# Optimization experiments

Hardware: AMD Instinct MI355X
Metric: run time of the kernel (lower is better)

Reference implementation:

```python
import jax, jax.numpy as jnp
import numpy as np

TIME_DIM = 2
DIM = 512
N_ENT = 100000
N_REL = 500
B = 512
K = 128
MARGIN = 2.0
EPS = 1e-6


def proj_tan0(u):
    # tangent space at origin o=(1,0,...,0): first coordinate zeroed
    return u.at[..., 0].set(0.0)


def expmap0(u):
    # exponential map at the origin of the pseudo-hyperboloid Q^{s,t}, beta=-1.
    # quadratic norm of tangent vector (time dims negative): branch on sign.
    u = proj_tan0(u)
    a = -jnp.sum(u[..., :TIME_DIM] ** 2, axis=-1) + jnp.sum(u[..., TIME_DIM:] ** 2, axis=-1)
    sp = jnp.sqrt(jnp.clip(a, EPS))   # space-like branch radius
    st = jnp.sqrt(jnp.clip(-a, EPS))  # time-like branch radius
    c = jnp.where(a > 0, jnp.cosh(sp), jnp.cos(st))
    s = jnp.where(a > 0, jnp.sinh(sp) / sp, jnp.sin(st) / st)
    o = jnp.zeros_like(u).at[..., 0].set(1.0)
    return c[..., None] * o + s[..., None] * u


def _norm_givens(r):
    g = r.reshape(r.shape[0], -1, 2)
    return g / jnp.clip(jnp.linalg.norm(g, axis=-1, keepdims=True), 1e-15)


def givens_rotations(r, x):
    g = _norm_givens(r)
    xp = x.reshape(r.shape[0], -1, 2)
    c, s = g[..., 0:1], g[..., 1:2]
    x0, x1 = xp[..., 0:1], xp[..., 1:2]
    out = jnp.concatenate([c * x0 - s * x1, c * x1 + s * x0], axis=-1)
    return out.reshape(r.shape[0], -1)


def givens_reflection(r, x):
    g = _norm_givens(r)
    xp = x.reshape(r.shape[0], -1, 2)
    c, s = g[..., 0:1], g[..., 1:2]
    x0, x1 = xp[..., 0:1], xp[..., 1:2]
    out = jnp.concatenate([c * x0 + s * x1, s * x0 - c * x1], axis=-1)
    return out.reshape(r.shape[0], -1)


def manhattan_sqdist(x, y):
    # Manhattan-style geodesic on Q^{s,t} via the S^{t-1} x H^s decomposition:
    # leg 1: rotate time direction on the sphere of radius ||x_t||,
    # leg 2: hyperbolic distance along the shared time direction. Asymmetric
    # in (x, y), hence the min over both orders in the caller.
    xt, xs = x[..., :TIME_DIM], x[..., TIME_DIM:]
    yt, ys = y[..., :TIME_DIM], y[..., TIME_DIM:]
    nx = jnp.linalg.norm(xt, axis=-1)
    ny = jnp.linalg.norm(yt, axis=-1)
    cosang = jnp.clip(jnp.sum(xt * yt, axis=-1) / (nx * ny), -1.0 + EPS, 1.0 - EPS)
    d_sph = nx * jnp.arccos(cosang)
    inner = nx * ny - jnp.sum(xs * ys, axis=-1)
    d_hyp = jnp.arccosh(jnp.clip(inner, 1.0 + EPS))
    return (d_sph + d_hyp) ** 2


def setup_inputs() -> dict:
    key = jax.random.key(0)
    ks = jax.random.split(key, 8)
    emb_entity = jax.random.normal(ks[0], (N_ENT, DIM), jnp.float32)
    relation_boost = 1e-5 * jax.nn.softplus(jax.random.normal(ks[1], (N_REL, TIME_DIM), jnp.float32))
    relation_rot_left = 2.0 * jax.random.uniform(ks[2], (N_REL, DIM), jnp.float32) - 1.0
    relation_rot_right = 2.0 * jax.random.uniform(ks[3], (N_REL, DIM), jnp.float32) - 1.0
    bias_head = jnp.zeros((N_ENT,), jnp.float32)
    bias_tail = jnp.zeros((N_ENT,), jnp.float32)
    u_idx = jax.random.randint(ks[4], (B,), 0, N_ENT)
    r_idx = jax.random.randint(ks[5], (B,), 0, N_REL)
    v_idx = jax.random.randint(ks[6], (B, K), 0, N_ENT)
    return {"emb_entity": emb_entity, "relation_boost": relation_boost,
            "relation_rot_left": relation_rot_left, "relation_rot_right": relation_rot_right,
            "bias_head": bias_head, "bias_tail": bias_tail,
            "u_idx": u_idx, "r_idx": r_idx, "v_idx": v_idx}


def reference(emb_entity, relation_boost, relation_rot_left, relation_rot_right,
              bias_head, bias_tail, u_idx, r_idx, v_idx):
    head = emb_entity[u_idx]                       # [B, D]
    tail = emb_entity[v_idx]                       # [B, K, D]
    b = jax.nn.softplus(relation_boost[r_idx])     # [B, 2]
    r_left = relation_rot_left[r_idx]
    r_right = relation_rot_right[r_idx]

    head = expmap0(head)
    tail = expmap0(proj_tan0(tail))

    head = givens_rotations(r_right, head)

    # dense (D x D) Lorentz boost per example, faithful to the original matmul
    C = jnp.sqrt(1.0 + b ** 2)
    t_idx = jnp.arange(TIME_DIM)
    bt_idx = DIM - TIME_DIM + jnp.arange(TIME_DIM)
    m_idx = jnp.arange(TIME_DIM, DIM - TIME_DIM)
    boost = jnp.zeros((b.shape[0], DIM, DIM), head.dtype)
    boost = boost.at[:, t_idx, t_idx].set(C)
    boost = boost.at[:, bt_idx, bt_idx].set(C)
    boost = boost.at[:, t_idx, bt_idx].set(-b)
    boost = boost.at[:, bt_idx, t_idx].set(-b)
    boost = boost.at[:, m_idx, m_idx].set(1.0)
    head = jnp.einsum('bij,bj->bi', boost, head)

    head = givens_reflection(r_left, head)

    # pairwise manifold distance, min over the two Manhattan-path orders
    c1 = manhattan_sqdist(head[:, None, :], tail)  # [B, K]
    c2 = manhattan_sqdist(tail, head[:, None, :])
    dist = jnp.minimum(c1, c2)

    return MARGIN - dist + bias_head[u_idx][:, None] + bias_tail[v_idx]
```

## Files before the change

kernel.cpp:

```cpp
#include <hip/hip_runtime.h>
#include <math.h>

#define DIM_ 512
#define K_ 128
#define EPS_ 1e-6f
#define MARGIN_ 2.0f
#define PI_ 3.14159265358979f
#define QSTRIDE 68

__device__ __forceinline__ float frcp(float x) { return __builtin_amdgcn_rcpf(x); }

__device__ __forceinline__ float fast_acos(float x) {
    float ax = fabsf(x);
    float p = -0.0187293f;
    p = p * ax + 0.0742610f;
    p = p * ax - 0.2121144f;
    p = p * ax + 1.5707288f;
    float r = sqrtf(fmaxf(1.f - ax, 0.f)) * p;
    return x < 0.f ? PI_ - r : r;
}

__device__ __forceinline__ void fast_coshsinh(float x, float& c, float& s) {
    float e  = __expf(x);
    float ei = frcp(e);
    c = 0.5f * (e + ei);
    s = 0.5f * (e - ei);
}

__device__ __forceinline__ void expmap_cs(float a, float& c, float& s) {
    if (a > 0.f) {
        float sp = sqrtf(fmaxf(a, EPS_));
        float ch, sh;
        fast_coshsinh(sp, ch, sh);
        c = ch; s = sh * frcp(sp);
    } else {
        float st = sqrtf(fmaxf(-a, EPS_));
        c = __cosf(st);
        s = __sinf(st) * frcp(st);
    }
}

__device__ __forceinline__ void givens_rot(float gc, float gs, float& x0, float& x1) {
    float rn = frcp(fmaxf(sqrtf(gc * gc + gs * gs), 1e-15f));
    float c = gc * rn, s = gs * rn;
    float y0 = c * x0 - s * x1;
    float y1 = c * x1 + s * x0;
    x0 = y0; x1 = y1;
}

__device__ __forceinline__ void givens_ref(float gc, float gs, float& x0, float& x1) {
    float rn = frcp(fmaxf(sqrtf(gc * gc + gs * gs), 1e-15f));
    float c = gc * rn, s = gs * rn;
    float y0 = c * x0 + s * x1;
    float y1 = s * x0 - c * x1;
    x0 = y0; x1 = y1;
}

__global__ __launch_bounds__(256) void ultrae_kernel(
    const float* __restrict__ emb,
    const float* __restrict__ rel_boost,
    const float* __restrict__ rot_left,
    const float* __restrict__ rot_right,
    const float* __restrict__ bias_head,
    const float* __restrict__ bias_tail,
    const int* __restrict__ u_idx,
    const int* __restrict__ r_idx,
    const int* __restrict__ v_idx,
    float* __restrict__ out)
{
    __shared__ float lds_q[4][8 * QSTRIDE + 4];
    __shared__ float lds_d[4][8 * QSTRIDE + 4];
    __shared__ float lds_t[4][8];

    const int b = blockIdx.x;
    const int lane = threadIdx.x & 63;
    const int wave = threadIdx.x >> 6;
    const int u = u_idx[b];
    const int r = r_idx[b];

    const int kbase = (blockIdx.y * 4 + wave) * 8;
    const int* vp = v_idx + b * K_ + kbase;
    const int4 vv0 = *(const int4*)(vp);
    const int4 vv1 = *(const int4*)(vp + 4);
    const int vi[8] = {vv0.x, vv0.y, vv0.z, vv0.w, vv1.x, vv1.y, vv1.z, vv1.w};
    float4 t0[8], t1[8];
#pragma unroll
    for (int j = 0; j < 8; ++j) {
        const float* trow = emb + (size_t)vi[j] * DIM_ + lane * 8;
        t0[j] = *(const float4*)trow;
        t1[j] = *(const float4*)(trow + 4);
    }

    const float* hrow = emb + (size_t)u * DIM_ + lane * 8;
    float4 h0 = *(const float4*)hrow;
    float4 h1 = *(const float4*)(hrow + 4);
    const float* rr = rot_right + (size_t)r * DIM_ + lane * 8;
    float4 gr0 = *(const float4*)rr;
    float4 gr1 = *(const float4*)(rr + 4);
    const float* rl = rot_left + (size_t)r * DIM_ + lane * 8;
    float4 gl0 = *(const float4*)rl;
    float4 gl1 = *(const float4*)(rl + 4);
    const float rb0 = rel_boost[2*r];
    const float rb1 = rel_boost[2*r+1];
    const float bh = bias_head[u];

    const int m = lane & 7;
    const int g = lane >> 3;
    float bt = 0.f;
    if (lane < 8) bt = bias_tail[vp[m]];

    if (lane == 0) h0.x = 0.f;
    float ps = h0.x*h0.x + h0.y*h0.y + h0.z*h0.z + h0.w*h0.w
             + h1.x*h1.x + h1.y*h1.y + h1.z*h1.z + h1.w*h1.w;
#pragma unroll
    for (int off = 32; off >= 1; off >>= 1) ps += __shfl_xor(ps, off, 64);
    float u1 = __shfl(h0.y, 0, 64);
    float a = ps - 2.f * u1 * u1;
    float ch, sh;
    expmap_cs(a, ch, sh);
    h0.x *= sh; h0.y *= sh; h0.z *= sh; h0.w *= sh;
    h1.x *= sh; h1.y *= sh; h1.z *= sh; h1.w *= sh;
    if (lane == 0) h0.x = ch;

    givens_rot(gr0.x, gr0.y, h0.x, h0.y);
    givens_rot(gr0.z, gr0.w, h0.z, h0.w);
    givens_rot(gr1.x, gr1.y, h1.x, h1.y);
    givens_rot(gr1.z, gr1.w, h1.z, h1.w);

    {
        float bb0 = __logf(1.f + __expf(rb0));
        float bb1 = __logf(1.f + __expf(rb1));
        float C0 = sqrtf(1.f + bb0*bb0);
        float C1 = sqrtf(1.f + bb1*bb1);
        float e0   = __shfl(h0.x, 0, 64);
        float e1   = __shfl(h0.y, 0, 64);
        float e510 = __shfl(h1.z, 63, 64);
        float e511 = __shfl(h1.w, 63, 64);
        if (lane == 0) {
            h0.x = C0*e0 - bb0*e510;
            h0.y = C1*e1 - bb1*e511;
        }
        if (lane == 63) {
            h1.z = C0*e510 - bb0*e0;
            h1.w = C1*e511 - bb1*e1;
        }
    }

    givens_ref(gl0.x, gl0.y, h0.x, h0.y);
    givens_ref(gl0.z, gl0.w, h0.z, h0.w);
    givens_ref(gl1.x, gl1.y, h1.x, h1.y);
    givens_ref(gl1.z, gl1.w, h1.z, h1.w);

    float hf0 = __shfl(h0.x, 0, 64);
    float hf1 = __shfl(h0.y, 0, 64);
    float nx = sqrtf(hf0*hf0 + hf1*hf1);
    if (lane == 0) { h0.x = 0.f; h0.y = 0.f; }
    const float rnx = frcp(nx);

    if (lane == 0) {
#pragma unroll
        for (int j = 0; j < 8; ++j) lds_t[wave][j] = t0[j].y;
    }

#pragma unroll
    for (int j = 0; j < 8; ++j) {
        float4 s0 = t0[j], s1 = t1[j];
        if (lane == 0) { s0.x = 0.f; s0.y = 0.f; }
        float qp = s0.x*s0.x + s0.y*s0.y + s0.z*s0.z + s0.w*s0.w
                 + s1.x*s1.x + s1.y*s1.y + s1.z*s1.z + s1.w*s1.w;
        float dp = h0.x*s0.x + h0.y*s0.y + h0.z*s0.z + h0.w*s0.w
                 + h1.x*s1.x + h1.y*s1.y + h1.z*s1.z + h1.w*s1.w;
        lds_q[wave][j * QSTRIDE + lane] = qp;
        lds_d[wave][j * QSTRIDE + lane] = dp;
    }

    __builtin_amdgcn_wave_barrier();

    float q = 0.f, d = 0.f;
    const float* qa = &lds_q[wave][m * QSTRIDE + g];
    const float* da = &lds_d[wave][m * QSTRIDE + g];
#pragma unroll
    for (int k = 0; k < 8; ++k) {
        q += qa[8 * k];
        d += da[8 * k];
    }
    q += __shfl_xor(q, 8, 64);  d += __shfl_xor(d, 8, 64);
    q += __shfl_xor(q, 16, 64); d += __shfl_xor(d, 16, 64);
    q += __shfl_xor(q, 32, 64); d += __shfl_xor(d, 32, 64);

    const float tt1 = lds_t[wave][m];

    float at = q - tt1 * tt1;
    float ct, st;
    expmap_cs(at, ct, st);
    float yt1 = st * tt1;
    float ny = sqrtf(ct*ct + yt1*yt1);
    float cosang = (hf0*ct + hf1*yt1) * rnx * frcp(ny);
    cosang = fminf(fmaxf(cosang, -1.f + EPS_), 1.f - EPS_);
    float dsph = fminf(nx, ny) * fast_acos(cosang);
    float inner = fmaxf(nx*ny - st*d, 1.f + EPS_);
    float dhyp = __logf(inner + sqrtf(inner - 1.f) * sqrtf(inner + 1.f));
    float dsum = dsph + dhyp;
    if (lane < 8) {
        out[b * K_ + kbase + m] = MARGIN_ - dsum*dsum + bh + bt;
    }
}

extern "C" void kernel_launch(void* const* d_in, const int* in_sizes, int n_in,
                              void* d_out, int out_size, void* d_ws, size_t ws_size,
                              hipStream_t stream) {
    const float* emb       = (const float*)d_in[0];
    const float* rel_boost = (const float*)d_in[1];
    const float* rot_left  = (const float*)d_in[2];
    const float* rot_right = (const float*)d_in[3];
    const float* bias_h    = (const float*)d_in[4];
    const float* bias_t    = (const float*)d_in[5];
    const int* u_idx       = (const int*)d_in[6];
    const int* r_idx       = (const int*)d_in[7];
    const int* v_idx       = (const int*)d_in[8];
    float* out = (float*)d_out;

    int B = in_sizes[6];
    dim3 grid(B, 4), block(256);
    hipLaunchKernelGGL(ultrae_kernel, grid, block, 0, stream,
                       emb, rel_boost, rot_left, rot_right,
                       bias_h, bias_t, u_idx, r_idx, v_idx, out);
}
```

Before: 272.7 us.

## Split head transform into a prep kernel and change per-lane element layout

The per-example head pipeline (expmap, Givens rotation, Lorentz boost, reflection) moves into a separate kernel that runs once per example. It writes the transformed head plus scalars (time components, norm, bias) to workspace, and the main kernel reads them. Before, each of the 16 waves handling an example recomputed the head. Lanes also now load two contiguous float4 chunks (offset lane*4 and +256) instead of eight adjacent floats, so each load instruction covers a contiguous span. The cost is an extra kernel launch and a workspace write/read round trip.

New measurement: 277.8 us. Within noise of the previous version (+1.9%).

```diff
diff --git a/kernel.cpp b/kernel.cpp
--- a/kernel.cpp
+++ b/kernel.cpp
@@ -7,6 +7,7 @@
 #define MARGIN_ 2.0f
 #define PI_ 3.14159265358979f
 #define QSTRIDE 68
+#define HSTRIDE 520
 
 __device__ __forceinline__ float frcp(float x) { return __builtin_amdgcn_rcpf(x); }
 
@@ -56,58 +57,36 @@
     x0 = y0; x1 = y1;
 }
 
-__global__ __launch_bounds__(256) void ultrae_kernel(
+__global__ __launch_bounds__(256) void head_prep(
     const float* __restrict__ emb,
     const float* __restrict__ rel_boost,
     const float* __restrict__ rot_left,
     const float* __restrict__ rot_right,
     const float* __restrict__ bias_head,
-    const float* __restrict__ bias_tail,
     const int* __restrict__ u_idx,
     const int* __restrict__ r_idx,
-    const int* __restrict__ v_idx,
-    float* __restrict__ out)
+    float* __restrict__ hws,
+    int B)
 {
-    __shared__ float lds_q[4][8 * QSTRIDE + 4];
-    __shared__ float lds_d[4][8 * QSTRIDE + 4];
-    __shared__ float lds_t[4][8];
-
-    const int b = blockIdx.x;
     const int lane = threadIdx.x & 63;
     const int wave = threadIdx.x >> 6;
+    const int b = blockIdx.x * 4 + wave;
+    if (b >= B) return;
     const int u = u_idx[b];
     const int r = r_idx[b];
 
-    const int kbase = (blockIdx.y * 4 + wave) * 8;
-    const int* vp = v_idx + b * K_ + kbase;
-    const int4 vv0 = *(const int4*)(vp);
-    const int4 vv1 = *(const int4*)(vp + 4);
-    const int vi[8] = {vv0.x, vv0.y, vv0.z, vv0.w, vv1.x, vv1.y, vv1.z, vv1.w};
-    float4 t0[8], t1[8];
-#pragma unroll
-    for (int j = 0; j < 8; ++j) {
-        const float* trow = emb + (size_t)vi[j] * DIM_ + lane * 8;
-        t0[j] = *(const float4*)trow;
-        t1[j] = *(const float4*)(trow + 4);
-    }
-
-    const float* hrow = emb + (size_t)u * DIM_ + lane * 8;
+    const float* hrow = emb + (size_t)u * DIM_ + lane * 4;
     float4 h0 = *(const float4*)hrow;
-    float4 h1 = *(const float4*)(hrow + 4);
-    const float* rr = rot_right + (size_t)r * DIM_ + lane * 8;
+    float4 h1 = *(const float4*)(hrow + 256);
+    const float* rr = rot_right + (size_t)r * DIM_ + lane * 4;
     float4 gr0 = *(const float4*)rr;
-    float4 gr1 = *(const float4*)(rr + 4);
-    const float* rl = rot_left + (size_t)r * DIM_ + lane * 8;
+    float4 gr1 = *(const float4*)(rr + 256);
+    const float* rl = rot_left + (size_t)r * DIM_ + lane * 4;
     float4 gl0 = *(const float4*)rl;
-    float4 gl1 = *(const float4*)(rl + 4);
+    float4 gl1 = *(const float4*)(rl + 256);
     const float rb0 = rel_boost[2*r];
     const float rb1 = rel_boost[2*r+1];
     const float bh = bias_head[u];
-
-    const int m = lane & 7;
-    const int g = lane >> 3;
-    float bt = 0.f;
-    if (lane < 8) bt = bias_tail[vp[m]];
 
     if (lane == 0) h0.x = 0.f;
     float ps = h0.x*h0.x + h0.y*h0.y + h0.z*h0.z + h0.w*h0.w
@@ -155,7 +134,54 @@
     float hf1 = __shfl(h0.y, 0, 64);
     float nx = sqrtf(hf0*hf0 + hf1*hf1);
     if (lane == 0) { h0.x = 0.f; h0.y = 0.f; }
-    const float rnx = frcp(nx);
+
+    float* o = hws + (size_t)b * HSTRIDE;
+    *(float4*)(o + lane * 4) = h0;
+    *(float4*)(o + 256 + lane * 4) = h1;
+    if (lane == 0) {
+        float4 sc = make_float4(hf0, hf1, nx, bh);
+        *(float4*)(o + 512) = sc;
+    }
+}
+
+__global__ __launch_bounds__(256) void ultrae_main(
+    const float* __restrict__ emb,
+    const float* __restrict__ bias_tail,
+    const int* __restrict__ v_idx,
+    const float* __restrict__ hws,
+    float* __restrict__ out)
+{
+    __shared__ float lds_q[4][8 * QSTRIDE + 4];
+    __shared__ float lds_d[4][8 * QSTRIDE + 4];
+    __shared__ float lds_t[4][8];
+
+    const int b = blockIdx.x;
+    const int lane = threadIdx.x & 63;
+    const int wave = threadIdx.x >> 6;
+
+    const int kbase = (blockIdx.y * 4 + wave) * 8;
+    const int* vp = v_idx + b * K_ + kbase;
+    const int4 vv0 = *(const int4*)(vp);
+    const int4 vv1 = *(const int4*)(vp + 4);
+
+    const float* hb = hws + (size_t)b * HSTRIDE;
+    float4 h0 = *(const float4*)(hb + lane * 4);
+    float4 h1 = *(const float4*)(hb + 256 + lane * 4);
+    const float4 sc = *(const float4*)(hb + 512);
+
+    const int vi[8] = {vv0.x, vv0.y, vv0.z, vv0.w, vv1.x, vv1.y, vv1.z, vv1.w};
+    float4 t0[8], t1[8];
+#pragma unroll
+    for (int j = 0; j < 8; ++j) {
+        const float* trow = emb + (size_t)vi[j] * DIM_ + lane * 4;
+        t0[j] = *(const float4*)trow;
+        t1[j] = *(const float4*)(trow + 256);
+    }
+
+    const int m = lane & 7;
+    const int g = lane >> 3;
+    float bt = 0.f;
+    if (lane < 8) bt = bias_tail[vp[m]];
 
     if (lane == 0) {
 #pragma unroll
@@ -190,6 +216,8 @@
 
     const float tt1 = lds_t[wave][m];
 
+    const float hf0 = sc.x, hf1 = sc.y, nx = sc.z, bh = sc.w;
+    const float rnx = frcp(nx);
     float at = q - tt1 * tt1;
     float ct, st;
     expmap_cs(at, ct, st);
@@ -219,10 +247,16 @@
     const int* r_idx       = (const int*)d_in[7];
     const int* v_idx       = (const int*)d_in[8];
     float* out = (float*)d_out;
+    float* hws = (float*)d_ws;
 
     int B = in_sizes[6];
+
+    dim3 gprep((B + 3) / 4), bprep(256);
+    hipLaunchKernelGGL(head_prep, gprep, bprep, 0, stream,
+                       emb, rel_boost, rot_left, rot_right,
+                       bias_h, u_idx, r_idx, hws, B);
+
     dim3 grid(B, 4), block(256);
-    hipLaunchKernelGGL(ultrae_kernel, grid, block, 0, stream,
-                       emb, rel_boost, rot_left, rot_right,
-                       bias_h, bias_t, u_idx, r_idx, v_idx, out);
-}
+    hipLaunchKernelGGL(ultrae_main, grid, block, 0, stream,
+                       emb, bias_t, v_idx, hws, out);
+}
```
